# Performance work log

Measured on AMD Instinct MI355X. Metric: run time of the kernel, lower is better.

Reference implementation:

```python
import jax, jax.numpy as jnp
import numpy as np

N, STATE_DIM, HID, D_EMB, K = 8192, 512, 128, 128, 10
EPS = 0.001


def setup_inputs() -> dict:
    key = jax.random.key(0)
    ks = jax.random.split(key, 5)
    sc = lambda fan_in: 1.0 / np.sqrt(fan_in)
    return {
        "s": jax.random.normal(ks[0], (N, STATE_DIM), dtype=jnp.float32),
        "W1": jax.random.normal(ks[1], (HID, STATE_DIM), dtype=jnp.float32) * sc(STATE_DIM),
        "b1": jax.random.normal(ks[2], (HID,), dtype=jnp.float32) * sc(STATE_DIM),
        "W2": jax.random.normal(ks[3], (D_EMB, HID), dtype=jnp.float32) * sc(HID),
        "b2": jax.random.normal(ks[4], (D_EMB,), dtype=jnp.float32) * sc(HID),
        "k": K,
    }


def reference(s, W1, b1, W2, b2, k):
    # embedding: relu(Linear) -> Linear
    x = jax.nn.relu(s @ W1.T + b1) @ W2.T + b2            # [N, d_emb]
    # pairwise L2 distance matrix: ||xi||^2 + ||xj||^2 - 2 xi.xj
    sq = jnp.sum(x * x, axis=1)                            # [N]
    dist2 = sq[:, None] + sq[None, :] - 2.0 * (x @ x.T)    # [N, N]
    # clamp tiny negative values from cancellation (torch.sqrt would NaN)
    dist = jnp.sqrt(jnp.maximum(dist2, 1e-12))             # [N, N]
    # k nearest per row, excluding self (smallest entry = own distance ~0)
    neg_vals, _ = jax.lax.top_k(-dist, k + 1)              # [N, k+1], ascending dist
    k_nearest = -neg_vals[:, 1:]                           # [N, k]
    sum_k_nearest = jnp.sum(k_nearest, axis=1, keepdims=True)  # [N, 1]
    mean_k_nearest_2 = jnp.mean(sum_k_nearest) ** 2
    return EPS / (sum_k_nearest ** 2 / mean_k_nearest_2 + EPS)
```

## Files before the change

kernel.cpp:

```cpp
#include <hip/hip_runtime.h>
#include <hip/hip_bf16.h>

#define NN 8192
#define SD 512
#define HID 128
#define DE 128
#define KP1 11
#define EPSF 0.001f
#define NSPLIT 32
#define NCHUNK NSPLIT
#define CB (NN / NSPLIT)
#define NSUB (CB / 16)
#define PBLK (8 * 2 * KP1 * 16)

using short8 = __attribute__((ext_vector_type(8))) short;
using f32x4 = __attribute__((ext_vector_type(4))) float;

__device__ inline ushort f2bf(float f) {
    __hip_bfloat16 b = __float2bfloat16(f);
    return *reinterpret_cast<ushort*>(&b);
}
__device__ inline float bf2f(ushort u) {
    unsigned v = (unsigned)u << 16;
    union { unsigned u; float f; } c; c.u = v; return c.f;
}

__global__ __launch_bounds__(256) void wsplit_kernel(
    const float* __restrict__ W1, const float* __restrict__ W2,
    ushort* __restrict__ W1h, ushort* __restrict__ W1l,
    ushort* __restrict__ W2h, ushort* __restrict__ W2l)
{
    const int bid = blockIdx.x;
    const float* src; ushort *dh, *dl; int base;
    if (bid < 64) { src = W1; dh = W1h; dl = W1l; base = bid * 1024; }
    else          { src = W2; dh = W2h; dl = W2l; base = (bid - 64) * 1024; }
    const int i = base + threadIdx.x * 4;
    float4 f = *reinterpret_cast<const float4*>(src + i);
    ushort h[4], lo[4];
    float fv[4] = {f.x, f.y, f.z, f.w};
#pragma unroll
    for (int j = 0; j < 4; ++j) {
        h[j] = f2bf(fv[j]);
        lo[j] = f2bf(fv[j] - bf2f(h[j]));
    }
    *reinterpret_cast<uint2*>(dh + i) = *reinterpret_cast<uint2*>(h);
    *reinterpret_cast<uint2*>(dl + i) = *reinterpret_cast<uint2*>(lo);
}

__global__ __launch_bounds__(512) void mlp_kernel(
    const float* __restrict__ s, const ushort* __restrict__ W1h,
    const ushort* __restrict__ W1l, const float* __restrict__ b1,
    const ushort* __restrict__ W2h, const ushort* __restrict__ W2l,
    const float* __restrict__ b2, __hip_bfloat16* __restrict__ xb,
    float* __restrict__ sqb)
{
    __shared__ __align__(16) ushort sbh[2][32 * 32];
    __shared__ __align__(16) ushort sbl[2][32 * 32];
    __shared__ __align__(16) ushort hbh[32 * 128];
    __shared__ __align__(16) ushort hbl[32 * 128];
    __shared__ __align__(16) ushort xtile[32 * 128];
    __shared__ float sqpart[8 * 32];

    const int t = threadIdx.x;
    const int w = t >> 6, l = t & 63;
    const int lc = l & 15, c4 = l >> 4;
    const int rb = blockIdx.x * 32;
    const int cb = w * 16;

    const int srow = t >> 4, sk = t & 15;
    const int ssl = ((sk >> 2) + (srow >> 2)) & 3;
    const int sByte = srow * 64 + (ssl ^ (srow & 3)) * 16 + (sk & 3) * 4;
    const float* sgbase = s + (size_t)(rb + srow) * SD + sk * 2;

    float2 sf;
#define STAGE_LOAD_S(kt_) sf = *reinterpret_cast<const float2*>(sgbase + (kt_) * 32)
#define STAGE_WRITE_S(b_) do { \
    ushort h0_ = f2bf(sf.x), h1_ = f2bf(sf.y); \
    ushort l0_ = f2bf(sf.x - bf2f(h0_)), l1_ = f2bf(sf.y - bf2f(h1_)); \
    *reinterpret_cast<unsigned*>(reinterpret_cast<char*>(sbh[b_]) + sByte) = \
        (unsigned)h0_ | ((unsigned)h1_ << 16); \
    *reinterpret_cast<unsigned*>(reinterpret_cast<char*>(sbl[b_]) + sByte) = \
        (unsigned)l0_ | ((unsigned)l1_ << 16); \
} while (0)

    int aByte[2];
#pragma unroll
    for (int rt = 0; rt < 2; ++rt) {
        int row = rt * 16 + lc;
        int sl = ((c4 + (row >> 2)) & 3) ^ (row & 3);
        aByte[rt] = row * 64 + sl * 16;
    }

    const int col = cb + lc;
    const ushort* w1hp = W1h + (size_t)col * SD + c4 * 8;
    const ushort* w1lp = W1l + (size_t)col * SD + c4 * 8;

    f32x4 acc1[2];
#pragma unroll
    for (int rt = 0; rt < 2; ++rt) acc1[rt] = {0.f, 0.f, 0.f, 0.f};

    STAGE_LOAD_S(0);
    STAGE_WRITE_S(0);
    short8 bh = *reinterpret_cast<const short8*>(w1hp);
    short8 bl = *reinterpret_cast<const short8*>(w1lp);
    short8 nbh, nbl;

    for (int kt = 0; kt < 16; ++kt) {
        __syncthreads();
        if (kt < 15) STAGE_LOAD_S(kt + 1);
        short8 ah[2], al[2];
#pragma unroll
        for (int rt = 0; rt < 2; ++rt) {
            ah[rt] = *reinterpret_cast<const short8*>(
                reinterpret_cast<char*>(sbh[kt & 1]) + aByte[rt]);
            al[rt] = *reinterpret_cast<const short8*>(
                reinterpret_cast<char*>(sbl[kt & 1]) + aByte[rt]);
        }
        if (kt < 15) {
            nbh = *reinterpret_cast<const short8*>(w1hp + (kt + 1) * 32);
            nbl = *reinterpret_cast<const short8*>(w1lp + (kt + 1) * 32);
        }
#pragma unroll
        for (int rt = 0; rt < 2; ++rt) {
            acc1[rt] = __builtin_amdgcn_mfma_f32_16x16x32_bf16(ah[rt], bh, acc1[rt], 0, 0, 0);
            acc1[rt] = __builtin_amdgcn_mfma_f32_16x16x32_bf16(ah[rt], bl, acc1[rt], 0, 0, 0);
            acc1[rt] = __builtin_amdgcn_mfma_f32_16x16x32_bf16(al[rt], bh, acc1[rt], 0, 0, 0);
        }
        if (kt < 15) {
            STAGE_WRITE_S((kt + 1) & 1);
            bh = nbh; bl = nbl;
        }
    }

    const float b1v = b1[col];
#pragma unroll
    for (int rt = 0; rt < 2; ++rt)
#pragma unroll
        for (int reg = 0; reg < 4; ++reg) {
            float v = fmaxf(acc1[rt][reg] + b1v, 0.f);
            ushort hh = f2bf(v);
            ushort hl = f2bf(v - bf2f(hh));
            int row = rt * 16 + c4 * 4 + reg;
            int sl = (col >> 3) ^ (row & 15);
            int byte = row * 256 + sl * 16 + (col & 7) * 2;
            *reinterpret_cast<ushort*>(reinterpret_cast<char*>(hbh) + byte) = hh;
            *reinterpret_cast<ushort*>(reinterpret_cast<char*>(hbl) + byte) = hl;
        }
    __syncthreads();

    f32x4 acc2[2];
#pragma unroll
    for (int rt = 0; rt < 2; ++rt) acc2[rt] = {0.f, 0.f, 0.f, 0.f};

#pragma unroll
    for (int kt = 0; kt < 4; ++kt) {
        short8 ah[2], al[2];
#pragma unroll
        for (int rt = 0; rt < 2; ++rt) {
            int row = rt * 16 + lc;
            int sl = (kt * 4 + c4) ^ (row & 15);
            int byte = row * 256 + sl * 16;
            ah[rt] = *reinterpret_cast<const short8*>(reinterpret_cast<char*>(hbh) + byte);
            al[rt] = *reinterpret_cast<const short8*>(reinterpret_cast<char*>(hbl) + byte);
        }
        short8 wh = *reinterpret_cast<const short8*>(W2h + (size_t)col * HID + kt * 32 + c4 * 8);
        short8 wl = *reinterpret_cast<const short8*>(W2l + (size_t)col * HID + kt * 32 + c4 * 8);
#pragma unroll
        for (int rt = 0; rt < 2; ++rt) {
            acc2[rt] = __builtin_amdgcn_mfma_f32_16x16x32_bf16(ah[rt], wh, acc2[rt], 0, 0, 0);
            acc2[rt] = __builtin_amdgcn_mfma_f32_16x16x32_bf16(ah[rt], wl, acc2[rt], 0, 0, 0);
            acc2[rt] = __builtin_amdgcn_mfma_f32_16x16x32_bf16(al[rt], wh, acc2[rt], 0, 0, 0);
        }
    }

    const float b2v = b2[col];
    float p[8];
#pragma unroll
    for (int j = 0; j < 8; ++j) p[j] = 0.f;
#pragma unroll
    for (int rt = 0; rt < 2; ++rt)
#pragma unroll
        for (int reg = 0; reg < 4; ++reg) {
            float v = acc2[rt][reg] + b2v;
            ushort xv = f2bf(v);
            float xf = bf2f(xv);
            p[rt * 4 + reg] = fmaf(xf, xf, p[rt * 4 + reg]);
            int row = rt * 16 + c4 * 4 + reg;
            xtile[row * 128 + col] = xv;
        }
#pragma unroll
    for (int j = 0; j < 8; ++j) {
#pragma unroll
        for (int off = 8; off >= 1; off >>= 1) p[j] += __shfl_xor(p[j], off, 16);
    }
    if (lc == 0) {
#pragma unroll
        for (int rt = 0; rt < 2; ++rt)
#pragma unroll
            for (int reg = 0; reg < 4; ++reg)
                sqpart[w * 32 + rt * 16 + c4 * 4 + reg] = p[rt * 4 + reg];
    }
    __syncthreads();
    if (t < 32) {
        float sq = 0.f;
#pragma unroll
        for (int ww = 0; ww < 8; ++ww) sq += sqpart[ww * 32 + t];
        sqb[rb + t] = sq;
    }
    const short8* xsv = reinterpret_cast<const short8*>(xtile);
    short8* xg = reinterpret_cast<short8*>(reinterpret_cast<ushort*>(xb) + (size_t)rb * DE);
    xg[t] = xsv[t];
}

__global__ __launch_bounds__(512) void knn_kernel(
    const ushort* __restrict__ xs, const float* __restrict__ sqb,
    float* __restrict__ part)
{
    __shared__ __align__(16) ushort lbuf[CB * DE];
    __shared__ __align__(16) float sqs[CB];

    const int bid = blockIdx.x;
    const int rid = bid >> 5, cid = bid & 31;
    const int t = threadIdx.x;
    const int w = t >> 6, l = t & 63;
    const int q16 = l & 15, lg = l >> 4;
    const int kk = lg * 8;
    const int qb = rid * 256 + w * 32;
    const int cstart = cid * CB;

    {
        const ushort* sb = xs + (size_t)cstart * DE;
#pragma unroll
        for (int i = 0; i < 8; ++i) {
            int sl = t + 512 * i;
            int row = sl >> 4, col = sl & 15;
            short8 v = *reinterpret_cast<const short8*>(sb + row * DE + col * 8);
            *reinterpret_cast<short8*>(&lbuf[(row * 16 + (col ^ (row & 7))) * 8]) = v;
        }
        if (t < 64)
            reinterpret_cast<float4*>(sqs)[t] =
                reinterpret_cast<const float4*>(sqb + cstart)[t];
    }

    short8 bq[2][4];
#pragma unroll
    for (int qs = 0; qs < 2; ++qs)
#pragma unroll
        for (int kb = 0; kb < 4; ++kb)
            bq[qs][kb] = *reinterpret_cast<const short8*>(
                xs + (size_t)(qb + qs * 16 + q16) * DE + kb * 32 + kk);

    float m[2][KP1];
#pragma unroll
    for (int qs = 0; qs < 2; ++qs)
#pragma unroll
        for (int j = 0; j < KP1; ++j) m[qs][j] = 1e30f;

#define INS(qs_, v_) do { \
    float d2_ = (v_); \
    _Pragma("unroll") \
    for (int j_ = KP1 - 1; j_ >= 1; --j_) \
        m[qs_][j_] = __builtin_amdgcn_fmed3f(d2_, m[qs_][j_ - 1], m[qs_][j_]); \
    m[qs_][0] = fminf(d2_, m[qs_][0]); \
} while (0)

    int aIdx[4];
#pragma unroll
    for (int kb = 0; kb < 4; ++kb)
        aIdx[kb] = (q16 * 16 + ((kb * 4 + lg) ^ (q16 & 7))) * 8;

    __syncthreads();

    short8 fa[4], fnext[4];
    float4 sv, svnext;
#pragma unroll
    for (int kb = 0; kb < 4; ++kb)
        fa[kb] = *reinterpret_cast<const short8*>(lbuf + aIdx[kb]);
    sv = *reinterpret_cast<const float4*>(sqs + lg * 4);

    for (int st = 0; st < NSUB; ++st) {
        if (st + 1 < NSUB) {
            const ushort* lbn = lbuf + (st + 1) * 2048;
#pragma unroll
            for (int kb = 0; kb < 4; ++kb)
                fnext[kb] = *reinterpret_cast<const short8*>(lbn + aIdx[kb]);
            svnext = *reinterpret_cast<const float4*>(sqs + (st + 1) * 16 + lg * 4);
        }
#pragma unroll
        for (int qs = 0; qs < 2; ++qs) {
            f32x4 acc = {0.f, 0.f, 0.f, 0.f};
#pragma unroll
            for (int kb = 0; kb < 4; ++kb)
                acc = __builtin_amdgcn_mfma_f32_16x16x32_bf16(fa[kb], bq[qs][kb], acc, 0, 0, 0);
            INS(qs, fmaf(-2.f, acc[0], sv.x));
            INS(qs, fmaf(-2.f, acc[1], sv.y));
            INS(qs, fmaf(-2.f, acc[2], sv.z));
            INS(qs, fmaf(-2.f, acc[3], sv.w));
        }
        if (st + 1 < NSUB) {
#pragma unroll
            for (int kb = 0; kb < 4; ++kb) fa[kb] = fnext[kb];
            sv = svnext;
        }
    }

    __syncthreads();
    float* mb = reinterpret_cast<float*>(lbuf);
#pragma unroll
    for (int qs = 0; qs < 2; ++qs)
#pragma unroll
        for (int j = 0; j < KP1; ++j)
            mb[(((w * 2 + qs) * 4 + lg) * KP1 + j) * 16 + q16] = m[qs][j];
    __syncthreads();
    if (l < 32) {
        const int qs = l >> 4, qq = l & 15;
        float mm[KP1];
#pragma unroll
        for (int j = 0; j < KP1; ++j)
            mm[j] = mb[(((w * 2 + qs) * 4 + 0) * KP1 + j) * 16 + qq];
#pragma unroll
        for (int g = 1; g < 4; ++g)
#pragma unroll
            for (int j = 0; j < KP1; ++j) {
                float d2 = mb[(((w * 2 + qs) * 4 + g) * KP1 + j) * 16 + qq];
#pragma unroll
                for (int jj = KP1 - 1; jj >= 1; --jj)
                    mm[jj] = __builtin_amdgcn_fmed3f(d2, mm[jj - 1], mm[jj]);
                mm[0] = fminf(d2, mm[0]);
            }
        float* pout = part + (size_t)bid * PBLK;
#pragma unroll
        for (int j = 0; j < KP1; ++j)
            pout[((w * 2 + qs) * KP1 + j) * 16 + qq] = mm[j];
    }
}

__global__ __launch_bounds__(256) void merge_kernel(
    const float* __restrict__ part, const float* __restrict__ sqb,
    float* __restrict__ sumk, float* __restrict__ psum)
{
    const int row = blockIdx.x * 256 + threadIdx.x;
    const int rid = row >> 8;
    const int sub = ((row >> 5) & 7) * 2 + ((row >> 4) & 1);
    const int lane = row & 15;
    const float* pbase = part + (size_t)rid * NSPLIT * PBLK + sub * (KP1 * 16) + lane;

    float m[KP1];
#pragma unroll
    for (int j = 0; j < KP1; ++j) m[j] = 1e30f;
#pragma unroll 4
    for (int ch = 0; ch < NCHUNK; ++ch) {
        const float* pc = pbase + ch * PBLK;
#pragma unroll
        for (int j = 0; j < KP1; ++j) {
            float d2 = pc[j * 16];
#pragma unroll
            for (int jj = KP1 - 1; jj >= 1; --jj)
                m[jj] = __builtin_amdgcn_fmed3f(d2, m[jj - 1], m[jj]);
            m[0] = fminf(d2, m[0]);
        }
    }
    const float sqq = sqb[row];
    float sum = 0.f;
#pragma unroll
    for (int j = 1; j < KP1; ++j)
        sum += sqrtf(fmaxf(m[j] + sqq, 1e-12f));
    sumk[row] = sum;

    float p = sum;
#pragma unroll
    for (int off = 32; off >= 1; off >>= 1) p += __shfl_xor(p, off, 64);
    __shared__ float red[4];
    if ((threadIdx.x & 63) == 0) red[threadIdx.x >> 6] = p;
    __syncthreads();
    if (threadIdx.x == 0) psum[blockIdx.x] = red[0] + red[1] + red[2] + red[3];
}

__global__ __launch_bounds__(256) void final_kernel(
    const float* __restrict__ sumk, const float* __restrict__ psum,
    float* __restrict__ out)
{
    __shared__ float qsh;
    const int t = threadIdx.x;
    if (t < 64) {
        float p = (t < 32) ? psum[t] : 0.f;
#pragma unroll
        for (int off = 32; off >= 1; off >>= 1) p += __shfl_xor(p, off, 64);
        if (t == 0) {
            float mean = p * (1.0f / NN);
            qsh = EPSF * mean * mean;
        }
    }
    __syncthreads();
    const float qq = qsh;
    const int i = blockIdx.x * 256 + t;
    const float sv = sumk[i];
    out[i] = qq / (fmaf(sv, sv, qq));
}

extern "C" void kernel_launch(void* const* d_in, const int* in_sizes, int n_in,
                              void* d_out, int out_size, void* d_ws, size_t ws_size,
                              hipStream_t stream)
{
    const float* s  = (const float*)d_in[0];
    const float* W1 = (const float*)d_in[1];
    const float* b1 = (const float*)d_in[2];
    const float* W2 = (const float*)d_in[3];
    const float* b2 = (const float*)d_in[4];
    float* out = (float*)d_out;

    char* ws = (char*)d_ws;
    __hip_bfloat16* xb = (__hip_bfloat16*)ws;
    float* sqb  = (float*)(ws + (size_t)NN * DE * 2);
    float* part = sqb + NN;
    float* sumk = part + (size_t)1024 * PBLK;
    float* psum = sumk + NN;
    ushort* W1h = (ushort*)(psum + 32);
    ushort* W1l = W1h + (size_t)HID * SD;
    ushort* W2h = W1l + (size_t)HID * SD;
    ushort* W2l = W2h + (size_t)DE * HID;

    wsplit_kernel<<<80, 256, 0, stream>>>(W1, W2, W1h, W1l, W2h, W2l);
    mlp_kernel<<<NN / 32, 512, 0, stream>>>(s, W1h, W1l, b1, W2h, W2l, b2, xb, sqb);
    knn_kernel<<<(NN / 256) * NSPLIT, 512, 0, stream>>>((const ushort*)xb, sqb, part);
    merge_kernel<<<NN / 256, 256, 0, stream>>>(part, sqb, sumk, psum);
    final_kernel<<<NN / 256, 256, 0, stream>>>(sumk, psum, out);
}
```

Measured before the change: 81.20 us.

## Parallelize top-k merge across lanes with shuffle butterfly; drop knn register prefetch

The merge kernel used to run one thread per row, each scanning all 32 partial top-k lists serially. It now gives each row 32 lanes, one per chunk, and merges the lists with a 5-step xor-shuffle butterfly, so it launches 1024 blocks instead of 32. The final kernel reduces 1024 partial sums instead of 32, and the workspace layout grows to match. The knn kernel's explicit double-buffered LDS prefetch is removed to simplify the loop and lower register pressure, which risks exposing LDS latency.

```diff
diff --git a/kernel.cpp b/kernel.cpp
--- a/kernel.cpp
+++ b/kernel.cpp
@@ -271,21 +271,13 @@
 
     __syncthreads();
 
-    short8 fa[4], fnext[4];
-    float4 sv, svnext;
-#pragma unroll
-    for (int kb = 0; kb < 4; ++kb)
-        fa[kb] = *reinterpret_cast<const short8*>(lbuf + aIdx[kb]);
-    sv = *reinterpret_cast<const float4*>(sqs + lg * 4);
-
     for (int st = 0; st < NSUB; ++st) {
-        if (st + 1 < NSUB) {
-            const ushort* lbn = lbuf + (st + 1) * 2048;
-#pragma unroll
-            for (int kb = 0; kb < 4; ++kb)
-                fnext[kb] = *reinterpret_cast<const short8*>(lbn + aIdx[kb]);
-            svnext = *reinterpret_cast<const float4*>(sqs + (st + 1) * 16 + lg * 4);
-        }
+        const ushort* lb = lbuf + st * 2048;
+        short8 fa[4];
+#pragma unroll
+        for (int kb = 0; kb < 4; ++kb)
+            fa[kb] = *reinterpret_cast<const short8*>(lb + aIdx[kb]);
+        float4 sv = *reinterpret_cast<const float4*>(sqs + st * 16 + lg * 4);
 #pragma unroll
         for (int qs = 0; qs < 2; ++qs) {
             f32x4 acc = {0.f, 0.f, 0.f, 0.f};
@@ -297,11 +289,6 @@
             INS(qs, fmaf(-2.f, acc[2], sv.z));
             INS(qs, fmaf(-2.f, acc[3], sv.w));
         }
-        if (st + 1 < NSUB) {
-#pragma unroll
-            for (int kb = 0; kb < 4; ++kb) fa[kb] = fnext[kb];
-            sv = svnext;
-        }
     }
 
     __syncthreads();
@@ -339,41 +326,51 @@
     const float* __restrict__ part, const float* __restrict__ sqb,
     float* __restrict__ sumk, float* __restrict__ psum)
 {
-    const int row = blockIdx.x * 256 + threadIdx.x;
+    __shared__ float rowsum[8];
+    const int t = threadIdx.x;
+    const int ww = t >> 6, l = t & 63;
+    const int half = l >> 5, c = l & 31;
+    const int row = blockIdx.x * 8 + ww * 2 + half;
     const int rid = row >> 8;
-    const int sub = ((row >> 5) & 7) * 2 + ((row >> 4) & 1);
-    const int lane = row & 15;
-    const float* pbase = part + (size_t)rid * NSPLIT * PBLK + sub * (KP1 * 16) + lane;
+    const int sub = (row >> 4) & 15;
+    const int qq = row & 15;
+    const float* pl = part + (size_t)(rid * 32 + c) * PBLK + sub * (KP1 * 16) + qq;
 
     float m[KP1];
 #pragma unroll
-    for (int j = 0; j < KP1; ++j) m[j] = 1e30f;
-#pragma unroll 4
-    for (int ch = 0; ch < NCHUNK; ++ch) {
-        const float* pc = pbase + ch * PBLK;
+    for (int j = 0; j < KP1; ++j) m[j] = pl[j * 16];
+
+#pragma unroll
+    for (int s = 1; s <= 16; s <<= 1) {
+        float o[KP1];
+#pragma unroll
+        for (int j = 0; j < KP1; ++j) o[j] = __shfl_xor(m[j], s, 64);
 #pragma unroll
         for (int j = 0; j < KP1; ++j) {
-            float d2 = pc[j * 16];
+            float d2 = o[j];
 #pragma unroll
             for (int jj = KP1 - 1; jj >= 1; --jj)
                 m[jj] = __builtin_amdgcn_fmed3f(d2, m[jj - 1], m[jj]);
             m[0] = fminf(d2, m[0]);
         }
     }
-    const float sqq = sqb[row];
-    float sum = 0.f;
-#pragma unroll
-    for (int j = 1; j < KP1; ++j)
-        sum += sqrtf(fmaxf(m[j] + sqq, 1e-12f));
-    sumk[row] = sum;
-
-    float p = sum;
-#pragma unroll
-    for (int off = 32; off >= 1; off >>= 1) p += __shfl_xor(p, off, 64);
-    __shared__ float red[4];
-    if ((threadIdx.x & 63) == 0) red[threadIdx.x >> 6] = p;
-    __syncthreads();
-    if (threadIdx.x == 0) psum[blockIdx.x] = red[0] + red[1] + red[2] + red[3];
+
+    if (c == 0) {
+        const float sqq = sqb[row];
+        float sum = 0.f;
+#pragma unroll
+        for (int j = 1; j < KP1; ++j)
+            sum += sqrtf(fmaxf(m[j] + sqq, 1e-12f));
+        sumk[row] = sum;
+        rowsum[ww * 2 + half] = sum;
+    }
+    __syncthreads();
+    if (t == 0) {
+        float p = 0.f;
+#pragma unroll
+        for (int i = 0; i < 8; ++i) p += rowsum[i];
+        psum[blockIdx.x] = p;
+    }
 }
 
 __global__ __launch_bounds__(256) void final_kernel(
@@ -381,15 +378,20 @@
     float* __restrict__ out)
 {
     __shared__ float qsh;
+    __shared__ float red[4];
     const int t = threadIdx.x;
-    if (t < 64) {
-        float p = (t < 32) ? psum[t] : 0.f;
+    {
+        float p = 0.f;
+#pragma unroll
+        for (int i = 0; i < 4; ++i) p += psum[t + i * 256];
 #pragma unroll
         for (int off = 32; off >= 1; off >>= 1) p += __shfl_xor(p, off, 64);
-        if (t == 0) {
-            float mean = p * (1.0f / NN);
-            qsh = EPSF * mean * mean;
-        }
+        if ((t & 63) == 0) red[t >> 6] = p;
+    }
+    __syncthreads();
+    if (t == 0) {
+        float mean = (red[0] + red[1] + red[2] + red[3]) * (1.0f / NN);
+        qsh = EPSF * mean * mean;
     }
     __syncthreads();
     const float qq = qsh;
@@ -415,7 +417,7 @@
     float* part = sqb + NN;
     float* sumk = part + (size_t)1024 * PBLK;
     float* psum = sumk + NN;
-    ushort* W1h = (ushort*)(psum + 32);
+    ushort* W1h = (ushort*)(psum + 1024);
     ushort* W1l = W1h + (size_t)HID * SD;
     ushort* W2h = W1l + (size_t)HID * SD;
     ushort* W2l = W2h + (size_t)DE * HID;
@@ -423,6 +425,6 @@
     wsplit_kernel<<<80, 256, 0, stream>>>(W1, W2, W1h, W1l, W2h, W2l);
     mlp_kernel<<<NN / 32, 512, 0, stream>>>(s, W1h, W1l, b1, W2h, W2l, b2, xb, sqb);
     knn_kernel<<<(NN / 256) * NSPLIT, 512, 0, stream>>>((const ushort*)xb, sqb, part);
-    merge_kernel<<<NN / 256, 256, 0, stream>>>(part, sqb, sumk, psum);
+    merge_kernel<<<NN / 8, 256, 0, stream>>>(part, sqb, sumk, psum);
     final_kernel<<<NN / 256, 256, 0, stream>>>(sumk, psum, out);
 }
```

After: 76.42 us, median of 2. 1.06x faster.
